# Kernel optimization log

Measured on AMD Instinct MI355X. Metric: run time of the kernel, lower is better.

## Reference

```python
import jax, jax.numpy as jnp
import numpy as np

B, LMAX, T_OUT, VOCAB, EMB, CVEC, HID, OUT = 8192, 12, 10, 36, 300, 256, 256, 512


def setup_inputs() -> dict:
    key = jax.random.key(0)
    ks = jax.random.split(key, 16)
    s = lambda fan: 1.0 / np.sqrt(fan)
    u = lambda k, shape, b: jax.random.uniform(k, shape, jnp.float32, -b, b)
    inp = {
        'words': jax.random.randint(ks[0], (B, LMAX), 0, VOCAB),
        'lengths': 1 + jax.random.randint(ks[1], (B,), 0, LMAX),  # in [1, LMAX]
        'emb_table': jax.random.normal(ks[2], (VOCAB, EMB), jnp.float32),
        'enc_w': u(ks[3], (CVEC, EMB), s(EMB)),
        'enc_b': u(ks[4], (CVEC,), s(EMB)),
        'wih_f': u(ks[5], (4 * HID, CVEC), s(HID)),
        'whh_f': u(ks[6], (4 * HID, HID), s(HID)),
        'bih_f': u(ks[7], (4 * HID,), s(HID)),
        'bhh_f': u(ks[8], (4 * HID,), s(HID)),
        'wih_b': u(ks[9], (4 * HID, CVEC), s(HID)),
        'whh_b': u(ks[10], (4 * HID, HID), s(HID)),
        'bih_b': u(ks[11], (4 * HID,), s(HID)),
        'bhh_b': u(ks[12], (4 * HID,), s(HID)),
        'out_w': u(ks[13], (OUT, 2 * HID), s(2 * HID)),
        'out_b': u(ks[14], (OUT,), s(2 * HID)),
    }
    return inp


def _interp_words(emb_table, words, lengths):
    # bilinear resize (L,300)->(10,300) with align_corners=True; width unchanged
    # so it is exact linear interpolation along the char axis.
    def one(word_row, L):
        Lf = (L - 1).astype(jnp.float32)
        pos = jnp.arange(T_OUT, dtype=jnp.float32) * Lf / (T_OUT - 1)  # (10,)
        i0 = jnp.floor(pos).astype(jnp.int32)
        i1 = jnp.minimum(i0 + 1, L - 1).astype(jnp.int32)
        f = (pos - i0.astype(jnp.float32))[:, None]
        e = emb_table[word_row]  # (LMAX, EMB)
        return e[i0] * (1.0 - f) + e[i1] * f  # (10, EMB)
    return jax.vmap(one)(words, lengths)  # (B, 10, EMB)


def _lstm(seq, wih, whh, bih, bhh):
    # seq: (T, B, In); PyTorch gate order i, f, g, o
    bsz = seq.shape[1]
    h0 = jnp.zeros((bsz, HID), seq.dtype)
    c0 = jnp.zeros((bsz, HID), seq.dtype)

    def step(carry, x_t):
        h, c = carry
        g = x_t @ wih.T + h @ whh.T + (bih + bhh)
        i, f, gg, o = jnp.split(g, 4, axis=-1)
        c = jax.nn.sigmoid(f) * c + jax.nn.sigmoid(i) * jnp.tanh(gg)
        h = jax.nn.sigmoid(o) * jnp.tanh(c)
        return (h, c), h

    _, hs = jax.lax.scan(step, (h0, c0), seq)
    return hs  # (T, B, HID)


def reference(words, lengths, emb_table, enc_w, enc_b, wih_f, whh_f, bih_f, bhh_f,
              wih_b, whh_b, bih_b, bhh_b, out_w, out_b):
    emb = _interp_words(emb_table, words, lengths)              # (B, 10, 300)
    cv = jax.nn.relu(emb @ enc_w.T + enc_b)                     # (B, 10, 256)
    seq = jnp.transpose(cv, (1, 0, 2))                          # (10, B, 256)
    h_f = _lstm(seq, wih_f, whh_f, bih_f, bhh_f)                # (10, B, 256)
    h_b = _lstm(seq[::-1], wih_b, whh_b, bih_b, bhh_b)[::-1]    # (10, B, 256)
    rec = jnp.concatenate([h_f, h_b], axis=-1)                  # (10, B, 512)
    out = rec @ out_w.T + out_b                                 # (10, B, 512)
    return jnp.transpose(out, (1, 0, 2))                        # (B, 10, 512)
```

## Files before the change

kernel.cpp:

```cpp
#include <hip/hip_runtime.h>
#include <hip/hip_fp16.h>

typedef _Float16 f16;
typedef _Float16 f16x2 __attribute__((ext_vector_type(2)));
typedef _Float16 f16x8 __attribute__((ext_vector_type(8)));
typedef float    f32x4 __attribute__((ext_vector_type(4)));

#define NB   8192
#define TOUT 10
#define LMAX 12
#define EMB  300

__device__ __forceinline__ float sigm_(float x) {
    return __builtin_amdgcn_rcpf(1.0f + __builtin_amdgcn_exp2f(x * -1.44269504f));
}
__device__ __forceinline__ float tanh_(float x) {
    return 1.0f - 2.0f * __builtin_amdgcn_rcpf(1.0f + __builtin_amdgcn_exp2f(x * 2.88539008f));
}
__device__ __forceinline__ f16x2 pk_f16(float a, float b) {
    return __builtin_bit_cast(f16x2, __builtin_amdgcn_cvt_pkrtz(a, b));
}

__global__ __launch_bounds__(256) void pack_w2(
    const float* __restrict__ wih_f, const float* __restrict__ whh_f,
    const float* __restrict__ wih_b, const float* __restrict__ whh_b,
    f16* __restrict__ Wp) {
    int idx = blockIdx.x * 256 + threadIdx.x;
    int d   = idx >> 19;
    int r   = idx & 524287;
    int tile = r >> 9;
    int e    = r & 511;
    int kc = tile >> 6, nt = tile & 63;
    int khi = e >> 7, rem = e & 127, nl = rem >> 3, klo = rem & 7;
    int n = nt * 16 + nl;
    int k = kc * 32 + khi * 8 + klo;
    int w = n >> 7, rr = n & 127, gate = rr >> 5;
    int u = w * 32 + 2 * (rr & 15) + ((rr >> 4) & 1);
    int srow = gate * 256 + u;
    const float* wih = d ? wih_b : wih_f;
    const float* whh = d ? whh_b : whh_f;
    float v = (k < 256) ? wih[srow * 256 + k] : whh[srow * 256 + (k - 256)];
    Wp[idx] = (f16)v;
}

__global__ __launch_bounds__(256) void pack_bias(
    const float* __restrict__ bih_f, const float* __restrict__ bhh_f,
    const float* __restrict__ bih_b, const float* __restrict__ bhh_b,
    float* __restrict__ bp) {
    int idx = blockIdx.x * 256 + threadIdx.x;
    int d = idx >> 10, n = idx & 1023;
    int w = n >> 7, rr = n & 127, gate = rr >> 5;
    int u = w * 32 + 2 * (rr & 15) + ((rr >> 4) & 1);
    int srow = gate * 256 + u;
    bp[idx] = d ? (bih_b[srow] + bhh_b[srow]) : (bih_f[srow] + bhh_f[srow]);
}

__global__ __launch_bounds__(256) void pack_w3(
    const float* __restrict__ out_w, f16* __restrict__ W3p) {
    int idx = blockIdx.x * 256 + threadIdx.x;
    int tile = idx >> 9, e = idx & 511;
    int kc = tile >> 5, nt = tile & 31;
    int khi = e >> 7, rem = e & 127, nl = rem >> 3, klo = rem & 7;
    int n = nt * 16 + nl, k = kc * 32 + khi * 8 + klo;
    W3p[idx] = (f16)out_w[n * 512 + k];
}

__global__ __launch_bounds__(256) void enc_proj(
    const float* __restrict__ tab, const float* __restrict__ ew,
    const float* __restrict__ eb, float* __restrict__ P) {
    int v = blockIdx.x, j = threadIdx.x;
    const float* a = tab + v * EMB;
    const float* w = ew + j * EMB;
    float s = 0.0f;
    for (int k = 0; k < EMB; ++k) s += a[k] * w[k];
    P[v * 256 + j] = s + eb[j];
}

__global__ __launch_bounds__(256) void build_seq(
    const int* __restrict__ words, const int* __restrict__ lengths,
    const float* __restrict__ P, f16* __restrict__ seqp) {
    int gi = blockIdx.x * 256 + threadIdx.x;
    int bl  = gi & 15;
    int khi = (gi >> 4) & 3;
    int kc  = (gi >> 6) & 7;
    int mt  = (gi >> 9) & 511;
    int t   = gi >> 18;
    int b = mt * 16 + bl;
    int L = lengths[b];
    float pos = ((float)t * (float)(L - 1)) / 9.0f;
    int i0 = (int)pos;
    float f = pos - (float)i0;
    int i1 = min(i0 + 1, L - 1);
    int c0 = words[b * LMAX + i0];
    int c1 = words[b * LMAX + i1];
    const float* p0 = P + c0 * 256 + kc * 32 + khi * 8;
    const float* p1 = P + c1 * 256 + kc * 32 + khi * 8;
    f16x8 r;
#pragma unroll
    for (int j = 0; j < 8; ++j) {
        float v = p0[j] * (1.0f - f) + p1[j] * f;
        v = fmaxf(v, 0.0f);
        r[j] = (f16)v;
    }
    *((f16x8*)seqp + gi) = r;
}

__global__ __launch_bounds__(512) void lstm_fused(
    const f16* __restrict__ seqp, const f16* __restrict__ Wp,
    const float* __restrict__ bp, f16* __restrict__ hcat) {
    const int dir  = blockIdx.x >> 7;
    const int r0t  = (blockIdx.x & 127) << 2;
    const int wave = threadIdx.x >> 6;
    const int lane = threadIdx.x & 63;
    const int l16  = lane & 15;
    const int quad = lane >> 4;

    __shared__ __align__(16) f16 hbuf[2][4 * 8 * 512];

    {
        f16x8 z = {(f16)0, (f16)0, (f16)0, (f16)0, (f16)0, (f16)0, (f16)0, (f16)0};
        for (int i = threadIdx.x; i < 2048; i += 512) ((f16x8*)hbuf[0])[i] = z;
    }

    const float* bpd = bp + dir * 1024 + wave * 128;
    float bias_l[8];
#pragma unroll
    for (int nt = 0; nt < 8; ++nt) bias_l[nt] = bpd[nt * 16 + l16];

    const f16* Wd = Wp + dir * 524288;

    const int wt0 = ((l16 >> 2) * 16 + quad * 4) * 8 + 2 * (l16 & 3);
    const int tile_lo = (r0t * 16 + dir * 8 + wave) * 512;

    float cst[4][4][2];
#pragma unroll
    for (int m = 0; m < 4; ++m)
#pragma unroll
        for (int q = 0; q < 4; ++q) { cst[m][q][0] = 0.0f; cst[m][q][1] = 0.0f; }

    __syncthreads();

    int cur = 0;
#pragma unroll 1
    for (int step = 0; step < TOUT; ++step) {
        const int t = dir ? (9 - step) : step;
        const f16* hb_r = hbuf[cur];
        f16*       hb_w = hbuf[cur ^ 1];

        f32x4 acc[4][8];
#pragma unroll
        for (int m = 0; m < 4; ++m)
#pragma unroll
            for (int nt = 0; nt < 8; ++nt)
#pragma unroll
                for (int q = 0; q < 4; ++q) acc[m][nt][q] = bias_l[nt];

        const f16* seqt = seqp + (size_t)(t * 512 + r0t) * 4096;

#pragma unroll 2
        for (int kc = 0; kc < 8; ++kc) {
            f16x8 bfrag[8];
#pragma unroll
            for (int nt = 0; nt < 8; ++nt)
                bfrag[nt] = *(const f16x8*)(Wd + ((kc * 64 + wave * 8 + nt) * 512 + lane * 8));
            f16x8 afrag[4];
#pragma unroll
            for (int m = 0; m < 4; ++m)
                afrag[m] = *(const f16x8*)(seqt + ((m * 8 + kc) * 512 + lane * 8));
#pragma unroll
            for (int m = 0; m < 4; ++m)
#pragma unroll
                for (int nt = 0; nt < 8; ++nt)
                    acc[m][nt] = __builtin_amdgcn_mfma_f32_16x16x32_f16(
                        afrag[m], bfrag[nt], acc[m][nt], 0, 0, 0);
        }
#pragma unroll 2
        for (int kcl = 0; kcl < 8; ++kcl) {
            int kc = kcl + 8;
            f16x8 bfrag[8];
#pragma unroll
            for (int nt = 0; nt < 8; ++nt)
                bfrag[nt] = *(const f16x8*)(Wd + ((kc * 64 + wave * 8 + nt) * 512 + lane * 8));
            f16x8 afrag[4];
#pragma unroll
            for (int m = 0; m < 4; ++m)
                afrag[m] = *(const f16x8*)(hb_r + ((m * 8 + kcl) * 512 + lane * 8));
#pragma unroll
            for (int m = 0; m < 4; ++m)
#pragma unroll
                for (int nt = 0; nt < 8; ++nt)
                    acc[m][nt] = __builtin_amdgcn_mfma_f32_16x16x32_f16(
                        afrag[m], bfrag[nt], acc[m][nt], 0, 0, 0);
        }

        f16* hct = hcat + ((size_t)t * 4194304 + tile_lo);
#pragma unroll
        for (int m = 0; m < 4; ++m) {
#pragma unroll
            for (int q = 0; q < 4; ++q) {
                float i0 = acc[m][0][q], i1 = acc[m][1][q];
                float f0 = acc[m][2][q], f1 = acc[m][3][q];
                float g0 = acc[m][4][q], g1 = acc[m][5][q];
                float o0 = acc[m][6][q], o1 = acc[m][7][q];
                float c0 = sigm_(f0) * cst[m][q][0] + sigm_(i0) * tanh_(g0);
                float c1 = sigm_(f1) * cst[m][q][1] + sigm_(i1) * tanh_(g1);
                cst[m][q][0] = c0;
                cst[m][q][1] = c1;
                float h0 = sigm_(o0) * tanh_(c0);
                float h1 = sigm_(o1) * tanh_(c1);
                f16x2 hv = pk_f16(h0, h1);
                int wt = wt0 + q * 8;
                *(f16x2*)&hb_w[(m * 8 + wave) * 512 + wt] = hv;
                *(f16x2*)(hct + m * 8192 + wt) = hv;
            }
        }

        __syncthreads();
        cur ^= 1;
    }
}

__global__ __launch_bounds__(512) void out_gemm(
    const f16* __restrict__ hcat, const f16* __restrict__ W3p,
    const float* __restrict__ out_b, float* __restrict__ out) {
    const int mt0  = blockIdx.x << 2;
    const int wave = threadIdx.x >> 6;
    const int lane = threadIdx.x & 63;
    const int l16  = lane & 15;
    const int quad = lane >> 4;
    const int n0   = wave * 64;

    float bias_l[4];
#pragma unroll
    for (int nt = 0; nt < 4; ++nt) bias_l[nt] = out_b[n0 + nt * 16 + l16];

    f32x4 acc[4][4];
#pragma unroll
    for (int m = 0; m < 4; ++m)
#pragma unroll
        for (int nt = 0; nt < 4; ++nt)
#pragma unroll
            for (int q = 0; q < 4; ++q) acc[m][nt][q] = bias_l[nt];

#pragma unroll 2
    for (int kc = 0; kc < 16; ++kc) {
        f16x8 a[4], b[4];
#pragma unroll
        for (int m = 0; m < 4; ++m)
            a[m] = *(const f16x8*)(hcat + ((size_t)((mt0 + m) * 16 + kc) * 512 + lane * 8));
#pragma unroll
        for (int nt = 0; nt < 4; ++nt)
            b[nt] = *(const f16x8*)(W3p + ((kc * 32 + wave * 4 + nt) * 512 + lane * 8));
#pragma unroll
        for (int m = 0; m < 4; ++m)
#pragma unroll
            for (int nt = 0; nt < 4; ++nt)
                acc[m][nt] = __builtin_amdgcn_mfma_f32_16x16x32_f16(a[m], b[nt], acc[m][nt], 0, 0, 0);
    }

#pragma unroll
    for (int m = 0; m < 4; ++m) {
#pragma unroll
        for (int nt = 0; nt < 4; ++nt) {
#pragma unroll
            for (int q = 0; q < 4; ++q) {
                int R = mt0 * 16 + m * 16 + quad * 4 + q;
                int t = R >> 13;
                int b = R & 8191;
                out[(size_t)(b * 10 + t) * 512 + n0 + nt * 16 + l16] = acc[m][nt][q];
            }
        }
    }
}

extern "C" void kernel_launch(void* const* d_in, const int* in_sizes, int n_in,
                              void* d_out, int out_size, void* d_ws, size_t ws_size,
                              hipStream_t stream) {
    const int*   words   = (const int*)d_in[0];
    const int*   lengths = (const int*)d_in[1];
    const float* tab     = (const float*)d_in[2];
    const float* enc_w   = (const float*)d_in[3];
    const float* enc_b   = (const float*)d_in[4];
    const float* wih_f   = (const float*)d_in[5];
    const float* whh_f   = (const float*)d_in[6];
    const float* bih_f   = (const float*)d_in[7];
    const float* bhh_f   = (const float*)d_in[8];
    const float* wih_b   = (const float*)d_in[9];
    const float* whh_b   = (const float*)d_in[10];
    const float* bih_b   = (const float*)d_in[11];
    const float* bhh_b   = (const float*)d_in[12];
    const float* out_w   = (const float*)d_in[13];
    const float* out_b   = (const float*)d_in[14];
    float* out = (float*)d_out;

    char* ws = (char*)d_ws;
    f16*   Wp   = (f16*)(ws + 0);
    f16*   W3p  = (f16*)(ws + 2097152);
    float* bp   = (float*)(ws + 2621440);
    float* P    = (float*)(ws + 2629632);
    f16*   seqp = (f16*)(ws + 2666496);
    f16*   hcat = (f16*)(ws + 44609536);

    pack_w2<<<4096, 256, 0, stream>>>(wih_f, whh_f, wih_b, whh_b, Wp);
    pack_bias<<<8, 256, 0, stream>>>(bih_f, bhh_f, bih_b, bhh_b, bp);
    pack_w3<<<1024, 256, 0, stream>>>(out_w, W3p);
    enc_proj<<<36, 256, 0, stream>>>(tab, enc_w, enc_b, P);
    build_seq<<<10240, 256, 0, stream>>>(words, lengths, P, seqp);
    lstm_fused<<<256, 512, 0, stream>>>(seqp, Wp, bp, hcat);
    out_gemm<<<1280, 512, 0, stream>>>(hcat, W3p, out_b, out);
}
```

Measured before the change: 476.4 us.

## Split LSTM gate tiles across 16 waves with 1024-thread blocks

Doubles the LSTM block to 1024 threads so each wave owns 64 gate columns (4 N-tiles, one per gate) instead of 128. The weight packing and bias order are remapped to match, and each lane now writes scalar f16 hidden values instead of packed pairs. The aim is more waves per CU to hide weight-load latency and cut per-wave accumulator registers. In exchange it adds narrower 2-byte stores and removes unrolling of the K loops, which may expose latency.

```diff
diff --git a/kernel.cpp b/kernel.cpp
--- a/kernel.cpp
+++ b/kernel.cpp
@@ -34,8 +34,8 @@
     int khi = e >> 7, rem = e & 127, nl = rem >> 3, klo = rem & 7;
     int n = nt * 16 + nl;
     int k = kc * 32 + khi * 8 + klo;
-    int w = n >> 7, rr = n & 127, gate = rr >> 5;
-    int u = w * 32 + 2 * (rr & 15) + ((rr >> 4) & 1);
+    int gate = (n >> 4) & 3;
+    int u = ((n >> 6) << 4) | (n & 15);
     int srow = gate * 256 + u;
     const float* wih = d ? wih_b : wih_f;
     const float* whh = d ? whh_b : whh_f;
@@ -49,8 +49,8 @@
     float* __restrict__ bp) {
     int idx = blockIdx.x * 256 + threadIdx.x;
     int d = idx >> 10, n = idx & 1023;
-    int w = n >> 7, rr = n & 127, gate = rr >> 5;
-    int u = w * 32 + 2 * (rr & 15) + ((rr >> 4) & 1);
+    int gate = (n >> 4) & 3;
+    int u = ((n >> 6) << 4) | (n & 15);
     int srow = gate * 256 + u;
     bp[idx] = d ? (bih_b[srow] + bhh_b[srow]) : (bih_f[srow] + bhh_f[srow]);
 }
@@ -105,7 +105,7 @@
     *((f16x8*)seqp + gi) = r;
 }
 
-__global__ __launch_bounds__(512) void lstm_fused(
+__global__ __launch_bounds__(1024) void lstm_fused(
     const f16* __restrict__ seqp, const f16* __restrict__ Wp,
     const float* __restrict__ bp, f16* __restrict__ hcat) {
     const int dir  = blockIdx.x >> 7;
@@ -119,24 +119,25 @@
 
     {
         f16x8 z = {(f16)0, (f16)0, (f16)0, (f16)0, (f16)0, (f16)0, (f16)0, (f16)0};
-        for (int i = threadIdx.x; i < 2048; i += 512) ((f16x8*)hbuf[0])[i] = z;
-    }
-
-    const float* bpd = bp + dir * 1024 + wave * 128;
-    float bias_l[8];
-#pragma unroll
-    for (int nt = 0; nt < 8; ++nt) bias_l[nt] = bpd[nt * 16 + l16];
-
-    const f16* Wd = Wp + dir * 524288;
-
-    const int wt0 = ((l16 >> 2) * 16 + quad * 4) * 8 + 2 * (l16 & 3);
-    const int tile_lo = (r0t * 16 + dir * 8 + wave) * 512;
-
-    float cst[4][4][2];
+        for (int i = threadIdx.x; i < 2048; i += 1024) ((f16x8*)hbuf[0])[i] = z;
+    }
+
+    const float* bpd = bp + dir * 1024 + wave * 64;
+    float bias_l[4];
+#pragma unroll
+    for (int nt = 0; nt < 4; ++nt) bias_l[nt] = bpd[nt * 16 + l16];
+
+    const f16* Wd = Wp + dir * 524288 + (wave * 4) * 512 + lane * 8;
+
+    const int slot = wave >> 1;
+    const int ofs0 = (((wave & 1) * 2 + (l16 >> 3)) * 16 + quad * 4) * 8 + (l16 & 7);
+    const int tile_lo = (r0t * 16 + dir * 8 + slot) * 512;
+
+    float cst[4][4];
 #pragma unroll
     for (int m = 0; m < 4; ++m)
 #pragma unroll
-        for (int q = 0; q < 4; ++q) { cst[m][q][0] = 0.0f; cst[m][q][1] = 0.0f; }
+        for (int q = 0; q < 4; ++q) cst[m][q] = 0.0f;
 
     __syncthreads();
 
@@ -144,51 +145,51 @@
 #pragma unroll 1
     for (int step = 0; step < TOUT; ++step) {
         const int t = dir ? (9 - step) : step;
-        const f16* hb_r = hbuf[cur];
+        const f16* hb_r = hbuf[cur] + lane * 8;
         f16*       hb_w = hbuf[cur ^ 1];
 
-        f32x4 acc[4][8];
+        f32x4 acc[4][4];
 #pragma unroll
         for (int m = 0; m < 4; ++m)
 #pragma unroll
-            for (int nt = 0; nt < 8; ++nt)
+            for (int nt = 0; nt < 4; ++nt)
 #pragma unroll
                 for (int q = 0; q < 4; ++q) acc[m][nt][q] = bias_l[nt];
 
-        const f16* seqt = seqp + (size_t)(t * 512 + r0t) * 4096;
-
-#pragma unroll 2
+        const f16* seqt = seqp + (size_t)(t * 512 + r0t) * 4096 + lane * 8;
+
+#pragma unroll 1
         for (int kc = 0; kc < 8; ++kc) {
-            f16x8 bfrag[8];
-#pragma unroll
-            for (int nt = 0; nt < 8; ++nt)
-                bfrag[nt] = *(const f16x8*)(Wd + ((kc * 64 + wave * 8 + nt) * 512 + lane * 8));
+            f16x8 bfrag[4];
+#pragma unroll
+            for (int nt = 0; nt < 4; ++nt)
+                bfrag[nt] = *(const f16x8*)(Wd + (kc * 64 + nt) * 512);
             f16x8 afrag[4];
 #pragma unroll
             for (int m = 0; m < 4; ++m)
-                afrag[m] = *(const f16x8*)(seqt + ((m * 8 + kc) * 512 + lane * 8));
+                afrag[m] = *(const f16x8*)(seqt + (m * 8 + kc) * 512);
 #pragma unroll
             for (int m = 0; m < 4; ++m)
 #pragma unroll
-                for (int nt = 0; nt < 8; ++nt)
+                for (int nt = 0; nt < 4; ++nt)
                     acc[m][nt] = __builtin_amdgcn_mfma_f32_16x16x32_f16(
                         afrag[m], bfrag[nt], acc[m][nt], 0, 0, 0);
         }
-#pragma unroll 2
+#pragma unroll 1
         for (int kcl = 0; kcl < 8; ++kcl) {
             int kc = kcl + 8;
-            f16x8 bfrag[8];
-#pragma unroll
-            for (int nt = 0; nt < 8; ++nt)
-                bfrag[nt] = *(const f16x8*)(Wd + ((kc * 64 + wave * 8 + nt) * 512 + lane * 8));
+            f16x8 bfrag[4];
+#pragma unroll
+            for (int nt = 0; nt < 4; ++nt)
+                bfrag[nt] = *(const f16x8*)(Wd + (kc * 64 + nt) * 512);
             f16x8 afrag[4];
 #pragma unroll
             for (int m = 0; m < 4; ++m)
-                afrag[m] = *(const f16x8*)(hb_r + ((m * 8 + kcl) * 512 + lane * 8));
+                afrag[m] = *(const f16x8*)(hb_r + (m * 8 + kcl) * 512);
 #pragma unroll
             for (int m = 0; m < 4; ++m)
 #pragma unroll
-                for (int nt = 0; nt < 8; ++nt)
+                for (int nt = 0; nt < 4; ++nt)
                     acc[m][nt] = __builtin_amdgcn_mfma_f32_16x16x32_f16(
                         afrag[m], bfrag[nt], acc[m][nt], 0, 0, 0);
         }
@@ -198,20 +199,16 @@
         for (int m = 0; m < 4; ++m) {
 #pragma unroll
             for (int q = 0; q < 4; ++q) {
-                float i0 = acc[m][0][q], i1 = acc[m][1][q];
-                float f0 = acc[m][2][q], f1 = acc[m][3][q];
-                float g0 = acc[m][4][q], g1 = acc[m][5][q];
-                float o0 = acc[m][6][q], o1 = acc[m][7][q];
-                float c0 = sigm_(f0) * cst[m][q][0] + sigm_(i0) * tanh_(g0);
-                float c1 = sigm_(f1) * cst[m][q][1] + sigm_(i1) * tanh_(g1);
-                cst[m][q][0] = c0;
-                cst[m][q][1] = c1;
-                float h0 = sigm_(o0) * tanh_(c0);
-                float h1 = sigm_(o1) * tanh_(c1);
-                f16x2 hv = pk_f16(h0, h1);
-                int wt = wt0 + q * 8;
-                *(f16x2*)&hb_w[(m * 8 + wave) * 512 + wt] = hv;
-                *(f16x2*)(hct + m * 8192 + wt) = hv;
+                float iv = acc[m][0][q];
+                float fv = acc[m][1][q];
+                float gv = acc[m][2][q];
+                float ov = acc[m][3][q];
+                float c = sigm_(fv) * cst[m][q] + sigm_(iv) * tanh_(gv);
+                cst[m][q] = c;
+                f16 hv = (f16)(sigm_(ov) * tanh_(c));
+                int wt = ofs0 + q * 8;
+                hb_w[(m * 8 + slot) * 512 + wt] = hv;
+                hct[m * 8192 + wt] = hv;
             }
         }
 
@@ -306,6 +303,6 @@
     pack_w3<<<1024, 256, 0, stream>>>(out_w, W3p);
     enc_proj<<<36, 256, 0, stream>>>(tab, enc_w, enc_b, P);
     build_seq<<<10240, 256, 0, stream>>>(words, lengths, P, seqp);
-    lstm_fused<<<256, 512, 0, stream>>>(seqp, Wp, bp, hcat);
+    lstm_fused<<<256, 1024, 0, stream>>>(seqp, Wp, bp, hcat);
     out_gemm<<<1280, 512, 0, stream>>>(hcat, W3p, out_b, out);
 }
```

After: 471.9 us. About the same (-0.9%).

## Prefetch next-step sequence input into LDS and software-pipeline weight fragment loads

Applied to the files above, without the earlier changes.

The LSTM kernel now asynchronously copies the next timestep's input tile into a double-buffered LDS buffer with global_load_lds, so it overlaps the current step's compute. The K loop is reordered to run the recurrent half first, and weight fragments are split into two half-sets that are prefetched one stage ahead, with s_setprio raised around the MFMA groups. This is meant to hide global-memory latency on the weight and activation loads. In exchange it doubles LDS use, which may reduce occupancy, and it relies on the existing barriers to order the async LDS writes.

```diff
diff --git a/kernel.cpp b/kernel.cpp
--- a/kernel.cpp
+++ b/kernel.cpp
@@ -19,6 +19,12 @@
 }
 __device__ __forceinline__ f16x2 pk_f16(float a, float b) {
     return __builtin_bit_cast(f16x2, __builtin_amdgcn_cvt_pkrtz(a, b));
+}
+
+__device__ __forceinline__ void gl_lds16(const f16* g, f16* l) {
+    __builtin_amdgcn_global_load_lds(
+        (const __attribute__((address_space(1))) void*)g,
+        (__attribute__((address_space(3))) void*)l, 16, 0, 0);
 }
 
 __global__ __launch_bounds__(256) void pack_w2(
@@ -115,19 +121,28 @@
     const int l16  = lane & 15;
     const int quad = lane >> 4;
 
-    __shared__ __align__(16) f16 hbuf[2][4 * 8 * 512];
+    __shared__ __align__(16) f16 hbuf[2][16384];
+    __shared__ __align__(16) f16 sbuf[2][16384];
 
     {
         f16x8 z = {(f16)0, (f16)0, (f16)0, (f16)0, (f16)0, (f16)0, (f16)0, (f16)0};
         for (int i = threadIdx.x; i < 2048; i += 512) ((f16x8*)hbuf[0])[i] = z;
     }
 
+    {
+        const int t0 = dir ? 9 : 0;
+        const f16* s0 = seqp + (size_t)(t0 * 512 + r0t) * 4096;
+#pragma unroll
+        for (int r = 0; r < 4; ++r)
+            gl_lds16(s0 + r * 4096 + threadIdx.x * 8, &sbuf[0][r * 4096 + wave * 512]);
+    }
+
     const float* bpd = bp + dir * 1024 + wave * 128;
     float bias_l[8];
 #pragma unroll
     for (int nt = 0; nt < 8; ++nt) bias_l[nt] = bpd[nt * 16 + l16];
 
-    const f16* Wd = Wp + dir * 524288;
+    const f16* Wdl = Wp + dir * 524288 + wave * 4096 + lane * 8;
 
     const int wt0 = ((l16 >> 2) * 16 + quad * 4) * 8 + 2 * (l16 & 3);
     const int tile_lo = (r0t * 16 + dir * 8 + wave) * 512;
@@ -144,9 +159,27 @@
 #pragma unroll 1
     for (int step = 0; step < TOUT; ++step) {
         const int t = dir ? (9 - step) : step;
-        const f16* hb_r = hbuf[cur];
+        const f16* hb_r = hbuf[cur] + lane * 8;
+        const f16* sb   = sbuf[cur] + lane * 8;
         f16*       hb_w = hbuf[cur ^ 1];
 
+        f16x8 bA[4], bB[4];
+#pragma unroll
+        for (int nt = 0; nt < 4; ++nt)
+            bA[nt] = *(const f16x8*)(Wdl + 8 * 32768 + nt * 512);
+#pragma unroll
+        for (int nt = 0; nt < 4; ++nt)
+            bB[nt] = *(const f16x8*)(Wdl + 8 * 32768 + (nt + 4) * 512);
+
+        if (step != 9) {
+            const int tn = dir ? (t - 1) : (t + 1);
+            const f16* ns = seqp + (size_t)(tn * 512 + r0t) * 4096;
+#pragma unroll
+            for (int r = 0; r < 4; ++r)
+                gl_lds16(ns + r * 4096 + threadIdx.x * 8,
+                         &sbuf[cur ^ 1][r * 4096 + wave * 512]);
+        }
+
         f32x4 acc[4][8];
 #pragma unroll
         for (int m = 0; m < 4; ++m)
@@ -155,42 +188,46 @@
 #pragma unroll
                 for (int q = 0; q < 4; ++q) acc[m][nt][q] = bias_l[nt];
 
-        const f16* seqt = seqp + (size_t)(t * 512 + r0t) * 4096;
-
-#pragma unroll 2
-        for (int kc = 0; kc < 8; ++kc) {
-            f16x8 bfrag[8];
-#pragma unroll
-            for (int nt = 0; nt < 8; ++nt)
-                bfrag[nt] = *(const f16x8*)(Wd + ((kc * 64 + wave * 8 + nt) * 512 + lane * 8));
-            f16x8 afrag[4];
+#pragma unroll 1
+        for (int j = 0; j < 16; ++j) {
+            const int c = j & 7;
+            const f16* ab = (j < 8) ? hb_r : sb;
+            f16x8 aA[4];
 #pragma unroll
             for (int m = 0; m < 4; ++m)
-                afrag[m] = *(const f16x8*)(seqt + ((m * 8 + kc) * 512 + lane * 8));
+                aA[m] = *(const f16x8*)(ab + (m * 8 + c) * 512);
+
+            __builtin_amdgcn_s_setprio(1);
 #pragma unroll
             for (int m = 0; m < 4; ++m)
 #pragma unroll
-                for (int nt = 0; nt < 8; ++nt)
+                for (int nt = 0; nt < 4; ++nt)
                     acc[m][nt] = __builtin_amdgcn_mfma_f32_16x16x32_f16(
-                        afrag[m], bfrag[nt], acc[m][nt], 0, 0, 0);
-        }
-#pragma unroll 2
-        for (int kcl = 0; kcl < 8; ++kcl) {
-            int kc = kcl + 8;
-            f16x8 bfrag[8];
-#pragma unroll
-            for (int nt = 0; nt < 8; ++nt)
-                bfrag[nt] = *(const f16x8*)(Wd + ((kc * 64 + wave * 8 + nt) * 512 + lane * 8));
-            f16x8 afrag[4];
+                        aA[m], bA[nt], acc[m][nt], 0, 0, 0);
+            __builtin_amdgcn_s_setprio(0);
+
+            if (j < 15) {
+                const int kcn = (j + 1) ^ 8;
+#pragma unroll
+                for (int nt = 0; nt < 4; ++nt)
+                    bA[nt] = *(const f16x8*)(Wdl + kcn * 32768 + nt * 512);
+            }
+
+            __builtin_amdgcn_s_setprio(1);
 #pragma unroll
             for (int m = 0; m < 4; ++m)
-                afrag[m] = *(const f16x8*)(hb_r + ((m * 8 + kcl) * 512 + lane * 8));
-#pragma unroll
-            for (int m = 0; m < 4; ++m)
-#pragma unroll
-                for (int nt = 0; nt < 8; ++nt)
-                    acc[m][nt] = __builtin_amdgcn_mfma_f32_16x16x32_f16(
-                        afrag[m], bfrag[nt], acc[m][nt], 0, 0, 0);
+#pragma unroll
+                for (int nt = 0; nt < 4; ++nt)
+                    acc[m][nt + 4] = __builtin_amdgcn_mfma_f32_16x16x32_f16(
+                        aA[m], bB[nt], acc[m][nt + 4], 0, 0, 0);
+            __builtin_amdgcn_s_setprio(0);
+
+            if (j < 15) {
+                const int kcn = (j + 1) ^ 8;
+#pragma unroll
+                for (int nt = 0; nt < 4; ++nt)
+                    bB[nt] = *(const f16x8*)(Wdl + kcn * 32768 + (nt + 4) * 512);
+            }
         }
 
         f16* hct = hcat + ((size_t)t * 4194304 + tile_lo);
```

Result: no change. 477.3 us (+0.2%).
